# Kernel optimization log

Hardware: AMD Instinct MI355X
Metric: run time of the kernel (lower is better)

## Reference

```python
import jax, jax.numpy as jnp
import numpy as np

# ---- static config (matches init_kwargs) ----
N, E = 8192, 262144
IN_CH, MP_CH, HID, K = 128, 512, 256, 10
EPS, DELTA = 1e-3, 0.311
TV_COEFF, BAL_COEFF = 0.785, 0.514


def setup_inputs() -> dict:
    key = jax.random.key(0)
    ks = jax.random.split(key, 16)

    def p(k, shape):
        fan_in = shape[0] if len(shape) > 1 else shape[0]
        return (jax.random.normal(k, shape, jnp.float32) / np.sqrt(fan_in)).astype(jnp.float32)

    return {
        "x": jax.random.normal(ks[0], (N, IN_CH), jnp.float32),
        "edge_index": jax.random.randint(ks[1], (2, E), 0, N, jnp.int32),
        "edge_weight": jax.random.uniform(ks[2], (E,), jnp.float32),
        # GTVConv layer 1 / 2 (Linear weight + bias)
        "W1": p(ks[3], (IN_CH, MP_CH)), "b1": jnp.zeros((MP_CH,), jnp.float32),
        "W2": p(ks[4], (MP_CH, MP_CH)), "b2": jnp.zeros((MP_CH,), jnp.float32),
        # pooling MLP [512 -> 256 -> K], relu, no norm
        "Wm1": p(ks[5], (MP_CH, HID)), "bm1": jnp.zeros((HID,), jnp.float32),
        "Wm2": p(ks[6], (HID, K)), "bm2": jnp.zeros((K,), jnp.float32),
    }


def _gtv_conv(x, src, dst, w, W, b):
    """GTVConv: out = elu( h - delta*(D_G h - Gamma h) + b ),
    gamma_ij = w_ij / max(||h_i - h_j||_1, eps), h = x @ W."""
    h = x @ W                                   # [N, C]
    diff = jnp.sum(jnp.abs(h[src] - h[dst]), axis=-1)   # [E]
    gamma = w / jnp.maximum(diff, EPS)                  # [E]
    deg = jnp.zeros(h.shape[0], h.dtype).at[dst].add(gamma)          # [N]
    agg = jnp.zeros_like(h).at[dst].add(gamma[:, None] * h[src])     # Gamma @ h
    out = h - DELTA * (deg[:, None] * h - agg) + b
    return jax.nn.elu(out)


def reference(x, edge_index, edge_weight, W1, b1, W2, b2, Wm1, bm1, Wm2, bm2):
    src, dst = edge_index[0], edge_index[1]

    h = _gtv_conv(x, src, dst, edge_weight, W1, b1)
    h = _gtv_conv(h, src, dst, edge_weight, W2, b2)

    # pooling MLP -> cluster logits s
    s_logits = jax.nn.relu(h @ Wm1 + bm1) @ Wm2 + bm2   # [N, K]

    # dense adjacency (to_dense_adj: duplicate edges accumulate)
    adj = jnp.zeros((N, N), x.dtype).at[src, dst].add(edge_weight)

    s = jax.nn.softmax(s_logits, axis=-1)

    # total-variation loss: sum_ij a_ij * sum_k |s_ik - s_jk| / (2 * nnz(adj))
    tv = jnp.zeros((), x.dtype)
    for k in range(K):  # small fixed loop over clusters, avoids [N,N,K] tensor
        col = s[:, k]
        tv = tv + jnp.sum(adj * jnp.abs(col[:, None] - col[None, :]))
    n_edges = jax.lax.stop_gradient(jnp.count_nonzero(adj).astype(x.dtype))
    tv = tv / (2.0 * n_edges)

    # asymmetric-norm balance loss (AsymCheegerCut)
    idx = N // K + 1                         # rho-quantile index (static)
    quant = jnp.sort(s, axis=0)[N - idx]     # idx-th largest per cluster, [K]
    t = s - quant[None, :]
    asym = jnp.where(t >= 0, (K - 1) * t, -t)
    denom = float(N * (K - 1))
    bal = (denom - jnp.sum(asym)) / denom

    return s_logits, TV_COEFF * tv, BAL_COEFF * bal
```

## Files before the change

kernel.cpp:

```cpp
#include <hip/hip_runtime.h>

#define N_NODES 8192
#define N_EDGES 262144
#define IN_CH 128
#define MP_CH 512
#define HID 256
#define KCL 10
#define EPS_C 0.001f
#define DELTA_C 0.311f
#define TV_COEFF_C 0.785f
#define BAL_COEFF_C 0.514f
#define RANK1 7373
#define DBINS 80

typedef __bf16 bf16x8 __attribute__((ext_vector_type(8)));
typedef float f32x4 __attribute__((ext_vector_type(4)));
typedef unsigned short ushort8 __attribute__((ext_vector_type(8)));

__device__ __forceinline__ float bf2f(unsigned short h) {
  union { unsigned int u; float f; } c; c.u = ((unsigned int)h) << 16; return c.f;
}
__device__ __forceinline__ unsigned short f2bf(float f) {
  union { float f; unsigned int u; } c; c.f = f;
  unsigned int r = c.u + 0x7fffu + ((c.u >> 16) & 1u);
  return (unsigned short)(r >> 16);
}

__global__ void prep_kernel(const float* __restrict__ x, const float* __restrict__ W1,
                            const float* __restrict__ W2, const float* __restrict__ Wm1,
                            unsigned short* __restrict__ xb, unsigned short* __restrict__ W1bt,
                            unsigned short* __restrict__ W2bt, unsigned short* __restrict__ Wm1bt,
                            const int* __restrict__ dst, int* __restrict__ cnt) {
  int i = blockIdx.x * 256 + threadIdx.x;
  if (i < 1048576) { xb[i] = f2bf(x[i]); return; }
  i -= 1048576;
  if (i < 65536) { int n = i >> 7, k = i & 127; W1bt[i] = f2bf(W1[k * MP_CH + n]); return; }
  i -= 65536;
  if (i < 262144) { int n = i >> 9, k = i & 511; W2bt[i] = f2bf(W2[k * MP_CH + n]); return; }
  i -= 262144;
  if (i < 131072) { int n = i >> 9, k = i & 511; Wm1bt[i] = f2bf(Wm1[k * HID + n]); return; }
  i -= 131072;
  if (i < N_EDGES) atomicAdd(&cnt[dst[i]], 1);
}

__global__ __launch_bounds__(1024) void scan_kernel(const int* __restrict__ cnt,
                                                    int* __restrict__ offs,
                                                    int* __restrict__ cursor,
                                                    int* __restrict__ nodeorder) {
  __shared__ int ts[1024];
  __shared__ int dh[DBINS];
  int t = threadIdx.x;
  int v[8]; int s = 0;
#pragma unroll
  for (int j = 0; j < 8; ++j) { v[j] = cnt[t * 8 + j]; s += v[j]; }
  if (t < DBINS) dh[t] = 0;
  ts[t] = s; __syncthreads();
  for (int off = 1; off < 1024; off <<= 1) {
    int add = (t >= off) ? ts[t - off] : 0;
    __syncthreads();
    ts[t] += add;
    __syncthreads();
  }
  int base = ts[t] - s;
#pragma unroll
  for (int j = 0; j < 8; ++j) {
    offs[t * 8 + j] = base; cursor[t * 8 + j] = base; base += v[j];
    int key = v[j] < (DBINS - 1) ? v[j] : (DBINS - 1);
    atomicAdd(&dh[(DBINS - 1) - key], 1);
  }
  if (t == 1023) offs[N_NODES] = ts[1023];
  __syncthreads();
  if (t == 0) {
    int acc0 = 0;
    for (int b = 0; b < DBINS; ++b) { int c = dh[b]; dh[b] = acc0; acc0 += c; }
  }
  __syncthreads();
#pragma unroll
  for (int j = 0; j < 8; ++j) {
    int key = v[j] < (DBINS - 1) ? v[j] : (DBINS - 1);
    int pos = atomicAdd(&dh[(DBINS - 1) - key], 1);
    nodeorder[pos] = t * 8 + j;
  }
}

__global__ void fill_kernel(const int* __restrict__ src, const int* __restrict__ dst,
                            const float* __restrict__ ew, int* __restrict__ cursor,
                            int2* __restrict__ esw) {
  for (int e = blockIdx.x * blockDim.x + threadIdx.x; e < N_EDGES; e += gridDim.x * blockDim.x) {
    int p = atomicAdd(&cursor[dst[e]], 1);
    esw[p] = make_int2(src[e], __float_as_int(ew[e]));
  }
}

__global__ __launch_bounds__(256) void gemm_bt(
    const unsigned short* __restrict__ A, const unsigned short* __restrict__ BT,
    float* __restrict__ C, unsigned short* __restrict__ Cb,
    const float* __restrict__ bias, int N, int K, int epi) {
  __shared__ unsigned short lsm[2 * 128 * 32];
  unsigned short* lA = lsm;
  unsigned short* lB = lsm + 128 * 32;
  int lane = threadIdx.x & 63;
  int wv = threadIdx.x >> 6;
  int tm = blockIdx.y * 128, tn = blockIdx.x * 128;
  int wm = (wv >> 1) * 64, wn = (wv & 1) * 64;
  int rA = lane & 15, quad = lane >> 4;
  f32x4 acc[4][4];
#pragma unroll
  for (int i = 0; i < 4; ++i)
#pragma unroll
    for (int j = 0; j < 4; ++j) acc[i][j] = (f32x4){0.f, 0.f, 0.f, 0.f};

  int arow = wv * 32 + (lane >> 2);
  int acol = (lane & 3) * 8;

  for (int k0 = 0; k0 < K; k0 += 32) {
#pragma unroll
    for (int c = 0; c < 2; ++c) {
      const unsigned short* ga = A + (size_t)(tm + arow + c * 16) * K + k0 + acol;
      __builtin_amdgcn_global_load_lds(
          (const __attribute__((address_space(1))) unsigned int*)ga,
          (__attribute__((address_space(3))) unsigned int*)(lA + (wv * 32 + c * 16) * 32),
          16, 0, 0);
      const unsigned short* gb = BT + (size_t)(tn + arow + c * 16) * K + k0 + acol;
      __builtin_amdgcn_global_load_lds(
          (const __attribute__((address_space(1))) unsigned int*)gb,
          (__attribute__((address_space(3))) unsigned int*)(lB + (wv * 32 + c * 16) * 32),
          16, 0, 0);
    }
    __syncthreads();
    bf16x8 af[4], bfr[4];
#pragma unroll
    for (int i = 0; i < 4; ++i)
      af[i] = *(const bf16x8*)(lA + (wm + i * 16 + rA) * 32 + quad * 8);
#pragma unroll
    for (int j = 0; j < 4; ++j)
      bfr[j] = *(const bf16x8*)(lB + (wn + j * 16 + rA) * 32 + quad * 8);
#pragma unroll
    for (int i = 0; i < 4; ++i)
#pragma unroll
      for (int j = 0; j < 4; ++j)
        acc[i][j] = __builtin_amdgcn_mfma_f32_16x16x32_bf16(af[i], bfr[j], acc[i][j], 0, 0, 0);
    __syncthreads();
  }

  if (epi == 1) {
#pragma unroll
    for (int i = 0; i < 4; ++i)
#pragma unroll
      for (int j = 0; j < 4; ++j)
#pragma unroll
        for (int r = 0; r < 4; ++r) {
          int row = tm + wm + i * 16 + quad * 4 + r;
          int col = tn + wn + j * 16 + rA;
          float v = acc[i][j][r] + bias[col];
          C[(size_t)row * N + col] = fmaxf(v, 0.f);
        }
  } else {
    float* fbuf = (float*)lsm;
    int band = threadIdx.x >> 7;
    int rrow = (threadIdx.x >> 3) & 15;
    int cg = threadIdx.x & 7;
#pragma unroll
    for (int i = 0; i < 4; ++i) {
#pragma unroll
      for (int j = 0; j < 4; ++j)
#pragma unroll
        for (int r = 0; r < 4; ++r)
          fbuf[(wv >> 1) * (16 * 128) + (quad * 4 + r) * 128 + (wn + j * 16 + rA)] =
              acc[i][j][r];
      __syncthreads();
      const float* sr = fbuf + band * (16 * 128) + rrow * 128 + cg * 16;
      unsigned short ov[16];
#pragma unroll
      for (int c = 0; c < 16; ++c) ov[c] = f2bf(sr[c]);
      size_t base = (size_t)(tm + band * 64 + i * 16 + rrow) * N + tn + cg * 16;
      *(ushort8*)(Cb + base) = *(ushort8*)ov;
      *(ushort8*)(Cb + base + 8) = *(ushort8*)(ov + 8);
      __syncthreads();
    }
  }
}

__global__ __launch_bounds__(256, 8) void gtv_node(
    const unsigned short* __restrict__ hb, const float* __restrict__ bias,
    const int2* __restrict__ esw, const int* __restrict__ offs,
    const int* __restrict__ nodeorder, unsigned short* __restrict__ outb) {
  __shared__ float sacc[2][MP_CH];
  int lane = threadIdx.x & 63;
  int wv = threadIdx.x >> 6;
  int pair = wv >> 1;
  int half = wv & 1;
  int d = __builtin_amdgcn_readfirstlane(nodeorder[blockIdx.x * 2 + pair]);
  ushort8 hdv = ((const ushort8*)(hb + (size_t)d * MP_CH))[lane];
  float hd[8], acc[8];
#pragma unroll
  for (int j = 0; j < 8; ++j) { hd[j] = bf2f(hdv[j]); acc[j] = 0.f; }
  int n0 = offs[d], n1 = offs[d + 1];
  int mid = n0 + ((n1 - n0 + 1) >> 1);
  int e0 = half ? mid : n0;
  int e1 = half ? n1 : mid;
  int i = e0;
  for (; i + 1 < e1; i += 2) {
    int2 ma = esw[i], mb = esw[i + 1];
    float wa = __int_as_float(ma.y), wb = __int_as_float(mb.y);
    ushort8 va = ((const ushort8*)(hb + (size_t)ma.x * MP_CH))[lane];
    ushort8 vb = ((const ushort8*)(hb + (size_t)mb.x * MP_CH))[lane];
    float pa = 0.f, pb = 0.f;
#pragma unroll
    for (int j = 0; j < 8; ++j) {
      pa += fabsf(hd[j] - bf2f(va[j]));
      pb += fabsf(hd[j] - bf2f(vb[j]));
    }
#pragma unroll
    for (int m = 1; m < 64; m <<= 1) { pa += __shfl_xor(pa, m, 64); pb += __shfl_xor(pb, m, 64); }
    float ga = wa * __builtin_amdgcn_rcpf(fmaxf(pa, EPS_C));
    float gb = wb * __builtin_amdgcn_rcpf(fmaxf(pb, EPS_C));
#pragma unroll
    for (int j = 0; j < 8; ++j)
      acc[j] += ga * (hd[j] - bf2f(va[j])) + gb * (hd[j] - bf2f(vb[j]));
  }
  if (i < e1) {
    int2 m0 = esw[i];
    float w = __int_as_float(m0.y);
    ushort8 sv = ((const ushort8*)(hb + (size_t)m0.x * MP_CH))[lane];
    float part = 0.f;
#pragma unroll
    for (int j = 0; j < 8; ++j) part += fabsf(hd[j] - bf2f(sv[j]));
#pragma unroll
    for (int m = 1; m < 64; m <<= 1) part += __shfl_xor(part, m, 64);
    float g = w * __builtin_amdgcn_rcpf(fmaxf(part, EPS_C));
#pragma unroll
    for (int j = 0; j < 8; ++j) acc[j] += g * (hd[j] - bf2f(sv[j]));
  }
  if (half) {
#pragma unroll
    for (int j = 0; j < 8; ++j) sacc[pair][lane * 8 + j] = acc[j];
  }
  __syncthreads();
  if (!half) {
    const f32x4* br = (const f32x4*)(bias + lane * 8);
    f32x4 b0 = br[0], b1 = br[1];
    unsigned short ov[8];
#pragma unroll
    for (int j = 0; j < 8; ++j) {
      float tot = acc[j] + sacc[pair][lane * 8 + j];
      float bv = (j < 4) ? b0[j] : b1[j - 4];
      float o = hd[j] - DELTA_C * tot + bv;
      o = (o > 0.f) ? o : (expf(o) - 1.f);
      ov[j] = f2bf(o);
    }
    *((ushort8*)(outb + (size_t)d * MP_CH) + lane) = *(ushort8*)ov;
  }
}

__global__ __launch_bounds__(256) void gemm_small(
    const float* __restrict__ hm, const float* __restrict__ W,
    const float* __restrict__ b, float* __restrict__ out, float* __restrict__ s) {
  __shared__ float lw[HID * KCL];
  __shared__ float lb[KCL];
  for (int i = threadIdx.x; i < HID * KCL; i += 256) lw[i] = W[i];
  if (threadIdx.x < KCL) lb[threadIdx.x] = b[threadIdx.x];
  __syncthreads();
  int lane = threadIdx.x & 63, wv = threadIdx.x >> 6;
  int row = blockIdx.x * 4 + wv;
  f32x4 hv = *(const f32x4*)(hm + (size_t)row * HID + lane * 4);
  float p[KCL];
#pragma unroll
  for (int n = 0; n < KCL; ++n) {
    int k0 = lane * 4;
    p[n] = hv[0] * lw[(k0 + 0) * KCL + n] + hv[1] * lw[(k0 + 1) * KCL + n] +
           hv[2] * lw[(k0 + 2) * KCL + n] + hv[3] * lw[(k0 + 3) * KCL + n];
  }
#pragma unroll
  for (int n = 0; n < KCL; ++n)
#pragma unroll
    for (int m = 1; m < 64; m <<= 1) p[n] += __shfl_xor(p[n], m, 64);
  if (lane == 0) {
    float vv[KCL]; float mx = -1e30f;
#pragma unroll
    for (int n = 0; n < KCL; ++n) {
      vv[n] = p[n] + lb[n];
      out[(size_t)row * KCL + n] = vv[n];
      mx = fmaxf(mx, vv[n]);
    }
    float sum = 0.f;
#pragma unroll
    for (int n = 0; n < KCL; ++n) { vv[n] = expf(vv[n] - mx); sum += vv[n]; }
    float inv = 1.f / sum;
#pragma unroll
    for (int n = 0; n < KCL; ++n) s[(size_t)row * KCL + n] = vv[n] * inv;
  }
}

__global__ __launch_bounds__(1024) void tvquant_kernel(
    const int* __restrict__ src, const int* __restrict__ dst,
    const float* __restrict__ ew, const float* __restrict__ s,
    unsigned int* __restrict__ bitmap, float* __restrict__ scal) {
  __shared__ float fsh[16];
  __shared__ int wcnt[2][16];
  int t = threadIdx.x;
  int lane = t & 63, wv = t >> 6;
  if (blockIdx.x < 246) {
    float local = 0.f;
    for (int e = blockIdx.x * 1024 + t; e < N_EDGES; e += 246 * 1024) {
      int a = src[e], b = dst[e];
      float w = ew[e];
      const float* sa = s + (size_t)a * KCL;
      const float* sb = s + (size_t)b * KCL;
      float tv = 0.f;
#pragma unroll
      for (int k = 0; k < KCL; ++k) tv += fabsf(sa[k] - sb[k]);
      local += w * tv;
      if (w != 0.f) {
        unsigned int key = ((unsigned int)a << 13) | (unsigned int)b;
        atomicOr(&bitmap[key >> 5], 1u << (key & 31u));
      }
    }
#pragma unroll
    for (int m = 1; m < 64; m <<= 1) local += __shfl_xor(local, m, 64);
    if (lane == 0) fsh[wv] = local;
    __syncthreads();
    if (t == 0) {
      float tot = 0.f;
#pragma unroll
      for (int i2 = 0; i2 < 16; ++i2) tot += fsh[i2];
      atomicAdd(&scal[0], tot);
    }
  } else {
    int k = blockIdx.x - 246;
    unsigned int v[8];
#pragma unroll
    for (int j = 0; j < 8; ++j)
      v[j] = __float_as_uint(s[(size_t)(t + j * 1024) * KCL + k]);
    unsigned int lo = 0u, hi = 0x3F800000u;
    int p = 0;
    while (lo < hi) {
      unsigned int mid = (lo + hi) >> 1;
      int c = 0;
#pragma unroll
      for (int j = 0; j < 8; ++j) c += (v[j] <= mid) ? 1 : 0;
#pragma unroll
      for (int m = 1; m < 64; m <<= 1) c += __shfl_xor(c, m, 64);
      if (lane == 0) wcnt[p][wv] = c;
      __syncthreads();
      int tot = 0;
#pragma unroll
      for (int i2 = 0; i2 < 16; ++i2) tot += wcnt[p][i2];
      if (tot >= RANK1) hi = mid; else lo = mid + 1;
      p ^= 1;
    }
    float q = __uint_as_float(lo);
    float local = 0.f;
#pragma unroll
    for (int j = 0; j < 8; ++j) {
      float tt = __uint_as_float(v[j]) - q;
      local += (tt >= 0.f) ? 9.f * tt : -tt;
    }
#pragma unroll
    for (int m = 1; m < 64; m <<= 1) local += __shfl_xor(local, m, 64);
    if (lane == 0) fsh[wv] = local;
    __syncthreads();
    if (t == 0) {
      float tot = 0.f;
#pragma unroll
      for (int i2 = 0; i2 < 16; ++i2) tot += fsh[i2];
      atomicAdd(&scal[1], tot);
    }
  }
}

__global__ __launch_bounds__(1024) void popcfin_kernel(const unsigned int* __restrict__ bm,
                                                       float* __restrict__ scal,
                                                       float* __restrict__ out) {
  __shared__ int ish[16];
  int t = threadIdx.x;
  int lane = t & 63, wv = t >> 6;
  int local = 0;
  for (int i = blockIdx.x * 1024 + t; i < (1 << 21); i += 256 * 1024)
    local += __popc(bm[i]);
#pragma unroll
  for (int m = 1; m < 64; m <<= 1) local += __shfl_xor(local, m, 64);
  if (lane == 0) ish[wv] = local;
  __syncthreads();
  if (t == 0) {
    int tot = 0;
#pragma unroll
    for (int i2 = 0; i2 < 16; ++i2) tot += ish[i2];
    atomicAdd((int*)(scal + 2), tot);
    __threadfence();
    int d = atomicAdd((int*)(scal + 3), 1);
    if (d == 255) {
      float tv = scal[0], asym = scal[1];
      float nedges = (float)(*(int*)(scal + 2));
      out[N_NODES * KCL] = TV_COEFF_C * (tv / (2.f * nedges));
      out[N_NODES * KCL + 1] = BAL_COEFF_C * ((73728.f - asym) / 73728.f);
    }
  }
}

#define OFF_BM     ((size_t)0)
#define OFF_CNT    ((size_t)8388608)
#define OFF_SCAL   ((size_t)8421376)
#define OFF_OFFS   ((size_t)8421888)
#define OFF_CURSOR ((size_t)8454912)
#define OFF_NORD   ((size_t)8487936)
#define OFF_HB     ((size_t)16777216)
#define OFF_OUTB   ((size_t)25165824)
#define OFF_HM     ((size_t)33554432)
#define OFF_XB     ((size_t)41943040)
#define OFF_W1BT   ((size_t)44040192)
#define OFF_W2BT   ((size_t)44171264)
#define OFF_WM1BT  ((size_t)44695552)
#define OFF_S      ((size_t)44957696)

extern "C" void kernel_launch(void* const* d_in, const int* in_sizes, int n_in,
                              void* d_out, int out_size, void* d_ws, size_t ws_size,
                              hipStream_t stream) {
  const float* x   = (const float*)d_in[0];
  const int*   ei  = (const int*)d_in[1];
  const float* ew  = (const float*)d_in[2];
  const float* W1  = (const float*)d_in[3];
  const float* b1  = (const float*)d_in[4];
  const float* W2  = (const float*)d_in[5];
  const float* b2  = (const float*)d_in[6];
  const float* Wm1 = (const float*)d_in[7];
  const float* bm1 = (const float*)d_in[8];
  const float* Wm2 = (const float*)d_in[9];
  const float* bm2 = (const float*)d_in[10];
  float* out = (float*)d_out;

  char* ws = (char*)d_ws;
  unsigned int*   bitmap = (unsigned int*)(ws + OFF_BM);
  int*            cnt    = (int*)(ws + OFF_CNT);
  float*          scal   = (float*)(ws + OFF_SCAL);
  int*            offs   = (int*)(ws + OFF_OFFS);
  int*            cursor = (int*)(ws + OFF_CURSOR);
  int*            nord   = (int*)(ws + OFF_NORD);
  unsigned short* hb     = (unsigned short*)(ws + OFF_HB);
  unsigned short* outb   = (unsigned short*)(ws + OFF_OUTB);
  float*          hm     = (float*)(ws + OFF_HM);
  int2*           esw    = (int2*)(ws + OFF_HM);
  unsigned short* xb     = (unsigned short*)(ws + OFF_XB);
  unsigned short* W1bt   = (unsigned short*)(ws + OFF_W1BT);
  unsigned short* W2bt   = (unsigned short*)(ws + OFF_W2BT);
  unsigned short* Wm1bt  = (unsigned short*)(ws + OFF_WM1BT);
  float*          s      = (float*)(ws + OFF_S);

  const int* srcA = ei;
  const int* dstA = ei + N_EDGES;

  hipMemsetAsync(ws, 0, 8421632, stream);

  prep_kernel<<<6912, 256, 0, stream>>>(x, W1, W2, Wm1, xb, W1bt, W2bt, Wm1bt, dstA, cnt);
  scan_kernel<<<1, 1024, 0, stream>>>(cnt, offs, cursor, nord);
  fill_kernel<<<1024, 256, 0, stream>>>(srcA, dstA, ew, cursor, esw);

  gemm_bt<<<dim3(MP_CH / 128, N_NODES / 128), 256, 0, stream>>>(
      xb, W1bt, nullptr, hb, nullptr, MP_CH, IN_CH, 2);
  gtv_node<<<N_NODES / 2, 256, 0, stream>>>(hb, b1, esw, offs, nord, outb);
  gemm_bt<<<dim3(MP_CH / 128, N_NODES / 128), 256, 0, stream>>>(
      outb, W2bt, nullptr, hb, nullptr, MP_CH, MP_CH, 2);
  gtv_node<<<N_NODES / 2, 256, 0, stream>>>(hb, b2, esw, offs, nord, outb);
  gemm_bt<<<dim3(HID / 128, N_NODES / 128), 256, 0, stream>>>(
      outb, Wm1bt, hm, nullptr, bm1, HID, MP_CH, 1);
  gemm_small<<<N_NODES / 4, 256, 0, stream>>>(hm, Wm2, bm2, out, s);

  tvquant_kernel<<<256, 1024, 0, stream>>>(srcA, dstA, ew, s, bitmap, scal);
  popcfin_kernel<<<256, 1024, 0, stream>>>(bitmap, scal, out);
}
```

Measured before the change: 258.8 us.

## Replace adjacency bitmap with CSR dedup count, fuse scan into prep and MLP head

Removes the 8 MB adjacency bitmap, its memset and the popcount kernel. Unique nonzero (src,dst) pairs are now counted by a per-destination duplicate scan over the CSR edge list. The single-block scan is folded into prep_kernel via a last-block-done counter, and the second MLP GEMM, ReLU, small GEMM and softmax are fused into one head kernel so the fp32 hidden buffer never goes to global memory. The dedup kernel adds a quadratic per-node pass, and the last-block scan runs serially at the tail of prep.

```diff
diff --git a/kernel.cpp b/kernel.cpp
--- a/kernel.cpp
+++ b/kernel.cpp
@@ -26,49 +26,49 @@
   return (unsigned short)(r >> 16);
 }
 
-__global__ void prep_kernel(const float* __restrict__ x, const float* __restrict__ W1,
-                            const float* __restrict__ W2, const float* __restrict__ Wm1,
-                            unsigned short* __restrict__ xb, unsigned short* __restrict__ W1bt,
-                            unsigned short* __restrict__ W2bt, unsigned short* __restrict__ Wm1bt,
-                            const int* __restrict__ dst, int* __restrict__ cnt) {
+__global__ __launch_bounds__(256) void prep_kernel(
+    const float* __restrict__ x, const float* __restrict__ W1,
+    const float* __restrict__ W2, const float* __restrict__ Wm1,
+    unsigned short* __restrict__ xb, unsigned short* __restrict__ W1bt,
+    unsigned short* __restrict__ W2bt, unsigned short* __restrict__ Wm1bt,
+    const int* __restrict__ dst, int* __restrict__ cnt,
+    int* __restrict__ offs, int* __restrict__ cursor,
+    int* __restrict__ nodeorder, int* __restrict__ scal_i) {
   int i = blockIdx.x * 256 + threadIdx.x;
-  if (i < 1048576) { xb[i] = f2bf(x[i]); return; }
-  i -= 1048576;
-  if (i < 65536) { int n = i >> 7, k = i & 127; W1bt[i] = f2bf(W1[k * MP_CH + n]); return; }
-  i -= 65536;
-  if (i < 262144) { int n = i >> 9, k = i & 511; W2bt[i] = f2bf(W2[k * MP_CH + n]); return; }
-  i -= 262144;
-  if (i < 131072) { int n = i >> 9, k = i & 511; Wm1bt[i] = f2bf(Wm1[k * HID + n]); return; }
-  i -= 131072;
-  if (i < N_EDGES) atomicAdd(&cnt[dst[i]], 1);
-}
-
-__global__ __launch_bounds__(1024) void scan_kernel(const int* __restrict__ cnt,
-                                                    int* __restrict__ offs,
-                                                    int* __restrict__ cursor,
-                                                    int* __restrict__ nodeorder) {
-  __shared__ int ts[1024];
+  if (i < 1048576) { xb[i] = f2bf(x[i]); }
+  else if ((i -= 1048576) < 65536) { int n = i >> 7, k = i & 127; W1bt[i] = f2bf(W1[k * MP_CH + n]); }
+  else if ((i -= 65536) < 262144) { int n = i >> 9, k = i & 511; W2bt[i] = f2bf(W2[k * MP_CH + n]); }
+  else if ((i -= 262144) < 131072) { int n = i >> 9, k = i & 511; Wm1bt[i] = f2bf(Wm1[k * HID + n]); }
+  else if ((i -= 131072) < N_EDGES) { atomicAdd(&cnt[dst[i]], 1); }
+
+  __shared__ int sdone;
+  __syncthreads();
+  if (threadIdx.x == 0) { __threadfence(); sdone = atomicAdd(&scal_i[8], 1); }
+  __syncthreads();
+  if (sdone != 6911) return;
+
+  __shared__ int ts[256];
   __shared__ int dh[DBINS];
   int t = threadIdx.x;
-  int v[8]; int s = 0;
-#pragma unroll
-  for (int j = 0; j < 8; ++j) { v[j] = cnt[t * 8 + j]; s += v[j]; }
+  int v[32]; int ssum = 0;
+#pragma unroll
+  for (int j = 0; j < 32; ++j) { v[j] = cnt[t * 32 + j]; ssum += v[j]; }
   if (t < DBINS) dh[t] = 0;
-  ts[t] = s; __syncthreads();
-  for (int off = 1; off < 1024; off <<= 1) {
+  ts[t] = ssum; __syncthreads();
+  for (int off = 1; off < 256; off <<= 1) {
     int add = (t >= off) ? ts[t - off] : 0;
     __syncthreads();
     ts[t] += add;
     __syncthreads();
   }
-  int base = ts[t] - s;
-#pragma unroll
-  for (int j = 0; j < 8; ++j) {
-    offs[t * 8 + j] = base; cursor[t * 8 + j] = base; base += v[j];
+  int base = ts[t] - ssum;
+#pragma unroll
+  for (int j = 0; j < 32; ++j) {
+    offs[t * 32 + j] = base; cursor[t * 32 + j] = base; base += v[j];
     int key = v[j] < (DBINS - 1) ? v[j] : (DBINS - 1);
     atomicAdd(&dh[(DBINS - 1) - key], 1);
   }
-  if (t == 1023) offs[N_NODES] = ts[1023];
+  if (t == 255) offs[N_NODES] = ts[255];
   __syncthreads();
   if (t == 0) {
     int acc0 = 0;
@@ -76,10 +76,10 @@
   }
   __syncthreads();
 #pragma unroll
-  for (int j = 0; j < 8; ++j) {
+  for (int j = 0; j < 32; ++j) {
     int key = v[j] < (DBINS - 1) ? v[j] : (DBINS - 1);
     int pos = atomicAdd(&dh[(DBINS - 1) - key], 1);
-    nodeorder[pos] = t * 8 + j;
+    nodeorder[pos] = t * 32 + j;
   }
 }
 
@@ -92,10 +92,33 @@
   }
 }
 
+__global__ __launch_bounds__(256) void dupcount_kernel(const int2* __restrict__ esw,
+                                                       const int* __restrict__ offs,
+                                                       float* __restrict__ scal) {
+  int lane = threadIdx.x & 63;
+  int wv = threadIdx.x >> 6;
+  int d = blockIdx.x * 4 + wv;
+  int n0 = offs[d], n1 = offs[d + 1];
+  int c = 0;
+  for (int bse = n0; bse < n1; bse += 64) {
+    int e = bse + lane;
+    int2 me = (e < n1) ? esw[e] : make_int2(-1, 0);
+    bool act = (e < n1) && (me.y != 0);
+    bool isnew = act;
+    int jend = (bse + 64 < n1) ? (bse + 64) : n1;
+    for (int j = n0; j < jend; ++j) {
+      int2 ej = esw[j];
+      if (act && j < e && ej.y != 0 && ej.x == me.x) isnew = false;
+    }
+    unsigned long long b = __ballot(isnew);
+    if (lane == 0) c += __popcll(b);
+  }
+  if (lane == 0 && c) atomicAdd((int*)(scal + 2), c);
+}
+
 __global__ __launch_bounds__(256) void gemm_bt(
     const unsigned short* __restrict__ A, const unsigned short* __restrict__ BT,
-    float* __restrict__ C, unsigned short* __restrict__ Cb,
-    const float* __restrict__ bias, int N, int K, int epi) {
+    unsigned short* __restrict__ Cb, int N, int K) {
   __shared__ unsigned short lsm[2 * 128 * 32];
   unsigned short* lA = lsm;
   unsigned short* lB = lsm + 128 * 32;
@@ -143,41 +166,27 @@
     __syncthreads();
   }
 
-  if (epi == 1) {
-#pragma unroll
-    for (int i = 0; i < 4; ++i)
-#pragma unroll
-      for (int j = 0; j < 4; ++j)
-#pragma unroll
-        for (int r = 0; r < 4; ++r) {
-          int row = tm + wm + i * 16 + quad * 4 + r;
-          int col = tn + wn + j * 16 + rA;
-          float v = acc[i][j][r] + bias[col];
-          C[(size_t)row * N + col] = fmaxf(v, 0.f);
-        }
-  } else {
-    float* fbuf = (float*)lsm;
-    int band = threadIdx.x >> 7;
-    int rrow = (threadIdx.x >> 3) & 15;
-    int cg = threadIdx.x & 7;
-#pragma unroll
-    for (int i = 0; i < 4; ++i) {
-#pragma unroll
-      for (int j = 0; j < 4; ++j)
-#pragma unroll
-        for (int r = 0; r < 4; ++r)
-          fbuf[(wv >> 1) * (16 * 128) + (quad * 4 + r) * 128 + (wn + j * 16 + rA)] =
-              acc[i][j][r];
-      __syncthreads();
-      const float* sr = fbuf + band * (16 * 128) + rrow * 128 + cg * 16;
-      unsigned short ov[16];
-#pragma unroll
-      for (int c = 0; c < 16; ++c) ov[c] = f2bf(sr[c]);
-      size_t base = (size_t)(tm + band * 64 + i * 16 + rrow) * N + tn + cg * 16;
-      *(ushort8*)(Cb + base) = *(ushort8*)ov;
-      *(ushort8*)(Cb + base + 8) = *(ushort8*)(ov + 8);
-      __syncthreads();
-    }
+  float* fbuf = (float*)lsm;
+  int band = threadIdx.x >> 7;
+  int rrow = (threadIdx.x >> 3) & 15;
+  int cg = threadIdx.x & 7;
+#pragma unroll
+  for (int i = 0; i < 4; ++i) {
+#pragma unroll
+    for (int j = 0; j < 4; ++j)
+#pragma unroll
+      for (int r = 0; r < 4; ++r)
+        fbuf[(wv >> 1) * (16 * 128) + (quad * 4 + r) * 128 + (wn + j * 16 + rA)] =
+            acc[i][j][r];
+    __syncthreads();
+    const float* sr = fbuf + band * (16 * 128) + rrow * 128 + cg * 16;
+    unsigned short ov[16];
+#pragma unroll
+    for (int c = 0; c < 16; ++c) ov[c] = f2bf(sr[c]);
+    size_t gbase = (size_t)(tm + band * 64 + i * 16 + rrow) * N + tn + cg * 16;
+    *(ushort8*)(Cb + gbase) = *(ushort8*)ov;
+    *(ushort8*)(Cb + gbase + 8) = *(ushort8*)(ov + 8);
+    __syncthreads();
   }
 }
 
@@ -253,34 +262,102 @@
   }
 }
 
-__global__ __launch_bounds__(256) void gemm_small(
-    const float* __restrict__ hm, const float* __restrict__ W,
-    const float* __restrict__ b, float* __restrict__ out, float* __restrict__ s) {
-  __shared__ float lw[HID * KCL];
-  __shared__ float lb[KCL];
-  for (int i = threadIdx.x; i < HID * KCL; i += 256) lw[i] = W[i];
-  if (threadIdx.x < KCL) lb[threadIdx.x] = b[threadIdx.x];
+__global__ __launch_bounds__(256) void head_fused(
+    const unsigned short* __restrict__ A,
+    const unsigned short* __restrict__ BT,
+    const float* __restrict__ bm1v, const float* __restrict__ Wm2v,
+    const float* __restrict__ bm2v, float* __restrict__ out, float* __restrict__ s) {
+  __shared__ unsigned short lA[32 * 32];
+  __shared__ unsigned short lB[256 * 32];
+  __shared__ float hbuf[256 * 41];
+  __shared__ float lW2[HID * KCL];
+  __shared__ float lb1[HID];
+  __shared__ float lb2[KCL];
+  int t = threadIdx.x;
+  int lane = t & 63, wv = t >> 6;
+  int rA = lane & 15, quad = lane >> 4;
+  int m0 = blockIdx.x * 32;
+
+  for (int i2 = t; i2 < HID * KCL; i2 += 256) lW2[i2] = Wm2v[i2];
+  lb1[t < HID ? t : 0] = bm1v[t < HID ? t : 0];
+  if (t < KCL) lb2[t] = bm2v[t];
+
+  f32x4 acc[2][4];
+#pragma unroll
+  for (int i = 0; i < 2; ++i)
+#pragma unroll
+    for (int j = 0; j < 4; ++j) acc[i][j] = (f32x4){0.f, 0.f, 0.f, 0.f};
+
+  for (int k0 = 0; k0 < MP_CH; k0 += 32) {
+    if (wv < 2) {
+      int row = wv * 16 + (lane >> 2);
+      const unsigned short* ga = A + (size_t)(m0 + row) * MP_CH + k0 + (lane & 3) * 8;
+      __builtin_amdgcn_global_load_lds(
+          (const __attribute__((address_space(1))) unsigned int*)ga,
+          (__attribute__((address_space(3))) unsigned int*)(lA + (wv * 16) * 32), 16, 0, 0);
+    }
+#pragma unroll
+    for (int q = 0; q < 4; ++q) {
+      int idx = wv * 4 + q;
+      int row = idx * 16 + (lane >> 2);
+      const unsigned short* gb = BT + (size_t)row * MP_CH + k0 + (lane & 3) * 8;
+      __builtin_amdgcn_global_load_lds(
+          (const __attribute__((address_space(1))) unsigned int*)gb,
+          (__attribute__((address_space(3))) unsigned int*)(lB + (idx * 16) * 32), 16, 0, 0);
+    }
+    __syncthreads();
+    bf16x8 af[2], bfr[4];
+#pragma unroll
+    for (int i = 0; i < 2; ++i)
+      af[i] = *(const bf16x8*)(lA + (i * 16 + rA) * 32 + quad * 8);
+#pragma unroll
+    for (int j = 0; j < 4; ++j)
+      bfr[j] = *(const bf16x8*)(lB + (wv * 64 + j * 16 + rA) * 32 + quad * 8);
+#pragma unroll
+    for (int i = 0; i < 2; ++i)
+#pragma unroll
+      for (int j = 0; j < 4; ++j)
+        acc[i][j] = __builtin_amdgcn_mfma_f32_16x16x32_bf16(af[i], bfr[j], acc[i][j], 0, 0, 0);
+    __syncthreads();
+  }
+
+#pragma unroll
+  for (int i = 0; i < 2; ++i)
+#pragma unroll
+    for (int j = 0; j < 4; ++j)
+#pragma unroll
+      for (int r = 0; r < 4; ++r) {
+        int row = i * 16 + quad * 4 + r;
+        int col = wv * 64 + j * 16 + rA;
+        hbuf[col * 41 + row] = fmaxf(acc[i][j][r] + lb1[col], 0.f);
+      }
   __syncthreads();
-  int lane = threadIdx.x & 63, wv = threadIdx.x >> 6;
-  int row = blockIdx.x * 4 + wv;
-  f32x4 hv = *(const f32x4*)(hm + (size_t)row * HID + lane * 4);
+
+  int row = t >> 3, g = t & 7;
   float p[KCL];
 #pragma unroll
+  for (int n = 0; n < KCL; ++n) p[n] = 0.f;
+#pragma unroll
+  for (int k = 0; k < 32; ++k) {
+    int col = k * 8 + g;
+    float hv = hbuf[col * 41 + row];
+    const float* wr = lW2 + col * KCL;
+#pragma unroll
+    for (int n = 0; n < KCL; ++n) p[n] += hv * wr[n];
+  }
+#pragma unroll
   for (int n = 0; n < KCL; ++n) {
-    int k0 = lane * 4;
-    p[n] = hv[0] * lw[(k0 + 0) * KCL + n] + hv[1] * lw[(k0 + 1) * KCL + n] +
-           hv[2] * lw[(k0 + 2) * KCL + n] + hv[3] * lw[(k0 + 3) * KCL + n];
-  }
-#pragma unroll
-  for (int n = 0; n < KCL; ++n)
-#pragma unroll
-    for (int m = 1; m < 64; m <<= 1) p[n] += __shfl_xor(p[n], m, 64);
-  if (lane == 0) {
+    p[n] += __shfl_xor(p[n], 1, 64);
+    p[n] += __shfl_xor(p[n], 2, 64);
+    p[n] += __shfl_xor(p[n], 4, 64);
+  }
+  if (g == 0) {
     float vv[KCL]; float mx = -1e30f;
+    size_t gr = (size_t)(m0 + row);
 #pragma unroll
     for (int n = 0; n < KCL; ++n) {
-      vv[n] = p[n] + lb[n];
-      out[(size_t)row * KCL + n] = vv[n];
+      vv[n] = p[n] + lb2[n];
+      out[gr * KCL + n] = vv[n];
       mx = fmaxf(mx, vv[n]);
     }
     float sum = 0.f;
@@ -288,14 +365,14 @@
     for (int n = 0; n < KCL; ++n) { vv[n] = expf(vv[n] - mx); sum += vv[n]; }
     float inv = 1.f / sum;
 #pragma unroll
-    for (int n = 0; n < KCL; ++n) s[(size_t)row * KCL + n] = vv[n] * inv;
+    for (int n = 0; n < KCL; ++n) s[gr * KCL + n] = vv[n] * inv;
   }
 }
 
 __global__ __launch_bounds__(1024) void tvquant_kernel(
     const int* __restrict__ src, const int* __restrict__ dst,
     const float* __restrict__ ew, const float* __restrict__ s,
-    unsigned int* __restrict__ bitmap, float* __restrict__ scal) {
+    float* __restrict__ scal, float* __restrict__ out) {
   __shared__ float fsh[16];
   __shared__ int wcnt[2][16];
   int t = threadIdx.x;
@@ -311,10 +388,6 @@
 #pragma unroll
       for (int k = 0; k < KCL; ++k) tv += fabsf(sa[k] - sb[k]);
       local += w * tv;
-      if (w != 0.f) {
-        unsigned int key = ((unsigned int)a << 13) | (unsigned int)b;
-        atomicOr(&bitmap[key >> 5], 1u << (key & 31u));
-      }
     }
 #pragma unroll
     for (int m = 1; m < 64; m <<= 1) local += __shfl_xor(local, m, 64);
@@ -367,46 +440,27 @@
       atomicAdd(&scal[1], tot);
     }
   }
-}
-
-__global__ __launch_bounds__(1024) void popcfin_kernel(const unsigned int* __restrict__ bm,
-                                                       float* __restrict__ scal,
-                                                       float* __restrict__ out) {
-  __shared__ int ish[16];
-  int t = threadIdx.x;
-  int lane = t & 63, wv = t >> 6;
-  int local = 0;
-  for (int i = blockIdx.x * 1024 + t; i < (1 << 21); i += 256 * 1024)
-    local += __popc(bm[i]);
-#pragma unroll
-  for (int m = 1; m < 64; m <<= 1) local += __shfl_xor(local, m, 64);
-  if (lane == 0) ish[wv] = local;
-  __syncthreads();
   if (t == 0) {
-    int tot = 0;
-#pragma unroll
-    for (int i2 = 0; i2 < 16; ++i2) tot += ish[i2];
-    atomicAdd((int*)(scal + 2), tot);
     __threadfence();
-    int d = atomicAdd((int*)(scal + 3), 1);
-    if (d == 255) {
-      float tv = scal[0], asym = scal[1];
-      float nedges = (float)(*(int*)(scal + 2));
-      out[N_NODES * KCL] = TV_COEFF_C * (tv / (2.f * nedges));
+    int dn = atomicAdd((int*)(scal + 3), 1);
+    if (dn == 255) {
+      float tv = atomicAdd(&scal[0], 0.f);
+      float asym = atomicAdd(&scal[1], 0.f);
+      int ne = atomicAdd((int*)(scal + 2), 0);
+      out[N_NODES * KCL] = TV_COEFF_C * (tv / (2.f * (float)ne));
       out[N_NODES * KCL + 1] = BAL_COEFF_C * ((73728.f - asym) / 73728.f);
     }
   }
 }
 
-#define OFF_BM     ((size_t)0)
-#define OFF_CNT    ((size_t)8388608)
-#define OFF_SCAL   ((size_t)8421376)
-#define OFF_OFFS   ((size_t)8421888)
-#define OFF_CURSOR ((size_t)8454912)
-#define OFF_NORD   ((size_t)8487936)
+#define OFF_CNT    ((size_t)0)
+#define OFF_SCAL   ((size_t)32768)
+#define OFF_OFFS   ((size_t)33024)
+#define OFF_CURSOR ((size_t)65796)
+#define OFF_NORD   ((size_t)98564)
 #define OFF_HB     ((size_t)16777216)
 #define OFF_OUTB   ((size_t)25165824)
-#define OFF_HM     ((size_t)33554432)
+#define OFF_ESW    ((size_t)33554432)
 #define OFF_XB     ((size_t)41943040)
 #define OFF_W1BT   ((size_t)44040192)
 #define OFF_W2BT   ((size_t)44171264)
@@ -430,7 +484,6 @@
   float* out = (float*)d_out;
 
   char* ws = (char*)d_ws;
-  unsigned int*   bitmap = (unsigned int*)(ws + OFF_BM);
   int*            cnt    = (int*)(ws + OFF_CNT);
   float*          scal   = (float*)(ws + OFF_SCAL);
   int*            offs   = (int*)(ws + OFF_OFFS);
@@ -438,8 +491,7 @@
   int*            nord   = (int*)(ws + OFF_NORD);
   unsigned short* hb     = (unsigned short*)(ws + OFF_HB);
   unsigned short* outb   = (unsigned short*)(ws + OFF_OUTB);
-  float*          hm     = (float*)(ws + OFF_HM);
-  int2*           esw    = (int2*)(ws + OFF_HM);
+  int2*           esw    = (int2*)(ws + OFF_ESW);
   unsigned short* xb     = (unsigned short*)(ws + OFF_XB);
   unsigned short* W1bt   = (unsigned short*)(ws + OFF_W1BT);
   unsigned short* W2bt   = (unsigned short*)(ws + OFF_W2BT);
@@ -449,22 +501,18 @@
   const int* srcA = ei;
   const int* dstA = ei + N_EDGES;
 
-  hipMemsetAsync(ws, 0, 8421632, stream);
-
-  prep_kernel<<<6912, 256, 0, stream>>>(x, W1, W2, Wm1, xb, W1bt, W2bt, Wm1bt, dstA, cnt);
-  scan_kernel<<<1, 1024, 0, stream>>>(cnt, offs, cursor, nord);
+  hipMemsetAsync(ws, 0, 33024, stream);
+
+  prep_kernel<<<6912, 256, 0, stream>>>(x, W1, W2, Wm1, xb, W1bt, W2bt, Wm1bt, dstA, cnt,
+                                        offs, cursor, nord, (int*)scal);
   fill_kernel<<<1024, 256, 0, stream>>>(srcA, dstA, ew, cursor, esw);
-
-  gemm_bt<<<dim3(MP_CH / 128, N_NODES / 128), 256, 0, stream>>>(
-      xb, W1bt, nullptr, hb, nullptr, MP_CH, IN_CH, 2);
+  dupcount_kernel<<<N_NODES / 4, 256, 0, stream>>>(esw, offs, scal);
+
+  gemm_bt<<<dim3(MP_CH / 128, N_NODES / 128), 256, 0, stream>>>(xb, W1bt, hb, MP_CH, IN_CH);
   gtv_node<<<N_NODES / 2, 256, 0, stream>>>(hb, b1, esw, offs, nord, outb);
-  gemm_bt<<<dim3(MP_CH / 128, N_NODES / 128), 256, 0, stream>>>(
-      outb, W2bt, nullptr, hb, nullptr, MP_CH, MP_CH, 2);
+  gemm_bt<<<dim3(MP_CH / 128, N_NODES / 128), 256, 0, stream>>>(outb, W2bt, hb, MP_CH, MP_CH);
   gtv_node<<<N_NODES / 2, 256, 0, stream>>>(hb, b2, esw, offs, nord, outb);
-  gemm_bt<<<dim3(HID / 128, N_NODES / 128), 256, 0, stream>>>(
-      outb, Wm1bt, hm, nullptr, bm1, HID, MP_CH, 1);
-  gemm_small<<<N_NODES / 4, 256, 0, stream>>>(hm, Wm2, bm2, out, s);
-
-  tvquant_kernel<<<256, 1024, 0, stream>>>(srcA, dstA, ew, s, bitmap, scal);
-  popcfin_kernel<<<256, 1024, 0, stream>>>(bitmap, scal, out);
-}
+  head_fused<<<N_NODES / 32, 256, 0, stream>>>(outb, Wm1bt, bm1, Wm2, bm2, out, s);
+
+  tvquant_kernel<<<256, 1024, 0, stream>>>(srcA, dstA, ew, s, scal, out);
+}
```

After: 471.9 us. 1.82x slower.
